# Optimization experiments

Hardware: AMD Instinct MI355X
Metric: run time of the kernel (lower is better)

## Reference

```python
import jax, jax.numpy as jnp
import numpy as np

B, C, H, W = 64, 768, 26, 26
M = 32
K_ATT = 192
NUM_CLASSES = 200
EPS = 1e-12


def setup_inputs() -> dict:
    key = jax.random.key(0)
    k1, k2, k3, k4, k5 = jax.random.split(key, 5)
    return {
        "feature_maps": jax.random.normal(k1, (B, C, H, W), dtype=jnp.float32),
        "att_w": jax.random.normal(k2, (K_ATT, C), dtype=jnp.float32) * 0.02,
        "att_b": jax.random.normal(k3, (K_ATT,), dtype=jnp.float32) * 0.02,
        "fc_w": jax.random.normal(k4, (NUM_CLASSES, M * C), dtype=jnp.float32) * 0.02,
        "fc_b": jax.random.normal(k5, (NUM_CLASSES,), dtype=jnp.float32) * 0.02,
    }


def reference(feature_maps, att_w, att_b, fc_w, fc_b):
    b, c, h, w = feature_maps.shape
    # 1x1 attention conv + relu, keep first M maps
    att = jax.nn.relu(
        jnp.einsum("bchw,kc->bkhw", feature_maps, att_w)
        + att_b[None, :, None, None]
    )
    att_m = att[:, :M]  # [B, M, H, W]

    # BAP: the Python loop multiply+avgpool+concat is a single batched contraction
    fm = jnp.einsum("bmhw,bchw->bmc", att_m, feature_maps) / (h * w)
    # signed sqrt
    fm = jnp.sign(fm) * jnp.sqrt(jnp.abs(fm) + EPS)
    # L2 normalize over dims (1, 2), matching F.normalize(eps=1e-12)
    nrm = jnp.sqrt(jnp.sum(fm * fm, axis=(1, 2), keepdims=True))
    fm = fm / jnp.maximum(nrm, EPS)

    # fc 1x1 conv on [B, M*C, 1, 1] == dense GEMM; input scaled by 100
    p = (fm.reshape(b, M * c) * 100.0) @ fc_w.T + fc_b
    return p, fm, att_m
```

## Files before the change

kernel.cpp:

```cpp
#include <hip/hip_runtime.h>
#include <hip/hip_bf16.h>


typedef unsigned short u16;
typedef __bf16 bf16x8_t __attribute__((ext_vector_type(8)));
typedef float f32x4_t __attribute__((ext_vector_type(4)));
typedef unsigned int uint32x4 __attribute__((ext_vector_type(4)));

union Frag { uint32x4 u4; unsigned u[4]; u16 s[8]; bf16x8_t v; };
union BFU { __hip_bfloat16 h; u16 u; };

__device__ inline u16 f2b(float x) { BFU t; t.h = __float2bfloat16(x); return t.u; }

__device__ inline void load8_cvt(const float* p, Frag& f) {
    f32x4_t x0 = *(const f32x4_t*)(p);
    f32x4_t x1 = *(const f32x4_t*)(p + 4);
#pragma unroll
    for (int j = 0; j < 4; ++j) { f.s[j] = f2b(x0[j]); f.s[4 + j] = f2b(x1[j]); }
}

#define MFMA(a, b, c) __builtin_amdgcn_mfma_f32_16x16x32_bf16((a), (b), (c), 0, 0, 0)

__global__ __launch_bounds__(256) void k_att(
    const float* __restrict__ fm, const float* __restrict__ att_w,
    const float* __restrict__ att_b, float* __restrict__ att_out,
    __hip_bfloat16* __restrict__ att_pad, float* __restrict__ p_sums)
{
    const int b  = blockIdx.y;
    const int p0 = blockIdx.x << 5;
    const int t  = threadIdx.x;
    const int wv = t >> 6, l = t & 63, q = l >> 4, ln = l & 15;

    if (blockIdx.x == 0 && t == 0) p_sums[b] = 0.f;

    __shared__ float red[32][32][4];

    f32x4_t acc[2][2] = {{{0.f,0.f,0.f,0.f},{0.f,0.f,0.f,0.f}},
                         {{0.f,0.f,0.f,0.f},{0.f,0.f,0.f,0.f}}};

    const int  kb   = wv * 192;
    const bool edge = (p0 == 672);
    const int  pb0  = p0 + ln;
    const int  pb1  = p0 + 16 + ln;

#pragma unroll
    for (int it = 0; it < 6; ++it) {
        const int k0 = kb + it * 32;
        Frag a0, a1, b0, b1;
        load8_cvt(att_w + (size_t)ln * 768 + k0 + q * 8, a0);
        load8_cvt(att_w + (size_t)(16 + ln) * 768 + k0 + q * 8, a1);
        const float* base = fm + (size_t)(b * 768 + k0 + q * 8) * 676;
        if (!edge) {
#pragma unroll
            for (int j = 0; j < 8; ++j) {
                b0.s[j] = f2b(base[(size_t)j * 676 + pb0]);
                b1.s[j] = f2b(base[(size_t)j * 676 + pb1]);
            }
        } else {
#pragma unroll
            for (int j = 0; j < 8; ++j) {
                b0.s[j] = (pb0 < 676) ? f2b(base[(size_t)j * 676 + pb0]) : (u16)0;
                b1.s[j] = (u16)0;
            }
        }
        acc[0][0] = MFMA(a0.v, b0.v, acc[0][0]);
        acc[0][1] = MFMA(a0.v, b1.v, acc[0][1]);
        acc[1][0] = MFMA(a1.v, b0.v, acc[1][0]);
        acc[1][1] = MFMA(a1.v, b1.v, acc[1][1]);
    }

#pragma unroll
    for (int mh = 0; mh < 2; ++mh)
#pragma unroll
        for (int ph = 0; ph < 2; ++ph)
#pragma unroll
            for (int r = 0; r < 4; ++r)
                red[mh * 16 + q * 4 + r][ph * 16 + ln][wv] = acc[mh][ph][r];
    __syncthreads();

    const int m = t >> 3, c0 = (t & 7) << 2;
#pragma unroll
    for (int j = 0; j < 4; ++j) {
        const int pl = c0 + j;
        f32x4_t v4 = *(const f32x4_t*)&red[m][pl][0];
        float v = v4[0] + v4[1] + v4[2] + v4[3] + att_b[m];
        v = v > 0.f ? v : 0.f;
        const int p = p0 + pl;
        BFU hb; hb.u = f2b(v);
        att_pad[(size_t)(b * 32 + m) * 704 + p] = (p < 676) ? hb.h : (__hip_bfloat16)0.f;
        if (p < 676)
            att_out[(size_t)(b * 32 + m) * 676 + p] = v;
    }
}

__global__ __launch_bounds__(256) void k_pool(
    const float* __restrict__ fm, const u16* __restrict__ att_pad,
    float* __restrict__ pooled, float* __restrict__ p_sums)
{
    const int b  = blockIdx.y;
    const int n0 = blockIdx.x << 5;
    const int t  = threadIdx.x;
    const int wv = t >> 6, l = t & 63, q = l >> 4, ln = l & 15;

    __shared__ float red[32][32][4];
    __shared__ float rs[4];

    const u16*   Ab = att_pad + (size_t)b * 32 * 704;
    const float* B0 = fm + (size_t)(b * 768 + n0 + ln) * 676;
    const float* B1 = fm + (size_t)(b * 768 + n0 + 16 + ln) * 676;

    f32x4_t acc[2][2] = {{{0.f,0.f,0.f,0.f},{0.f,0.f,0.f,0.f}},
                         {{0.f,0.f,0.f,0.f},{0.f,0.f,0.f,0.f}}};

    for (int it = wv; it < 22; it += 4) {
        const int k = it * 32 + q * 8;
        Frag a0, a1, b0, b1;
        a0.u4 = *(const uint32x4*)(Ab + (size_t)ln * 704 + k);
        a1.u4 = *(const uint32x4*)(Ab + (size_t)(16 + ln) * 704 + k);
        if (it < 21) {
            load8_cvt(B0 + k, b0);
            load8_cvt(B1 + k, b1);
        } else {
            b0.u[0]=0u; b0.u[1]=0u; b0.u[2]=0u; b0.u[3]=0u;
            b1.u[0]=0u; b1.u[1]=0u; b1.u[2]=0u; b1.u[3]=0u;
            if (q == 0) {
                f32x4_t x0 = *(const f32x4_t*)(B0 + 672);
                f32x4_t x1 = *(const f32x4_t*)(B1 + 672);
#pragma unroll
                for (int j = 0; j < 4; ++j) { b0.s[j] = f2b(x0[j]); b1.s[j] = f2b(x1[j]); }
            }
        }
        acc[0][0] = MFMA(a0.v, b0.v, acc[0][0]);
        acc[0][1] = MFMA(a0.v, b1.v, acc[0][1]);
        acc[1][0] = MFMA(a1.v, b0.v, acc[1][0]);
        acc[1][1] = MFMA(a1.v, b1.v, acc[1][1]);
    }

#pragma unroll
    for (int mh = 0; mh < 2; ++mh)
#pragma unroll
        for (int ch = 0; ch < 2; ++ch)
#pragma unroll
            for (int r = 0; r < 4; ++r)
                red[mh * 16 + q * 4 + r][ch * 16 + ln][wv] = acc[mh][ch][r];
    __syncthreads();

    const float sc = 1.0f / 676.0f;
    const int m = t >> 3, c0 = (t & 7) << 2;
    float ls = 0.f;
#pragma unroll
    for (int j = 0; j < 4; ++j) {
        const int cl = c0 + j;
        f32x4_t v4 = *(const f32x4_t*)&red[m][cl][0];
        float v = (v4[0] + v4[1] + v4[2] + v4[3]) * sc;
        pooled[(size_t)(b * 32 + m) * 768 + n0 + cl] = v;
        ls += fabsf(v);
    }
    for (int off = 32; off > 0; off >>= 1) ls += __shfl_down(ls, off);
    if (l == 0) rs[wv] = ls;
    __syncthreads();
    if (t == 0) atomicAdd(p_sums + b, rs[0] + rs[1] + rs[2] + rs[3]);
}

__global__ __launch_bounds__(256) void k_norm(
    const float* __restrict__ pooled, const float* __restrict__ p_sums,
    float* __restrict__ fm_out, u16* __restrict__ fmn16)
{
    const int b = blockIdx.x;
    const size_t base = (size_t)b * 24576 + (size_t)blockIdx.y * 2048;
    const float tot = p_sums[b] + 24576.f * 1e-12f;
    const float inv = 1.f / fmaxf(sqrtf(tot), 1e-12f);
    const int t = threadIdx.x;
#pragma unroll
    for (int i = 0; i < 8; ++i) {
        const size_t idx = base + i * 256 + t;
        float x = pooled[idx];
        float v = (x == 0.f) ? 0.f : copysignf(sqrtf(fabsf(x) + 1e-12f), x);
        float o = v * inv;
        fm_out[idx] = o;
        fmn16[idx]  = f2b(o);
    }
}

__global__ __launch_bounds__(256) void k_fc(
    const u16* __restrict__ fmn16, const float* __restrict__ fc_w,
    float* __restrict__ p_part)
{
    const int ntile = blockIdx.x;
    const int slab  = blockIdx.y;
    const int t = threadIdx.x;
    const int wv = t >> 6, l = t & 63, q = l >> 4, ln = l & 15;
    const int n = ntile * 16 + ln;
    const int kbase = slab * 512;

    const u16*   Ab = fmn16 + (size_t)(wv * 16 + ln) * 24576 + kbase + q * 8;
    const float* Bb = fc_w + (size_t)n * 24576 + kbase + q * 8;
    const bool nok = n < 200;

    f32x4_t acc = {0.f, 0.f, 0.f, 0.f};
#pragma unroll
    for (int kk = 0; kk < 512; kk += 32) {
        Frag af, bf2;
        af.u4 = *(const uint32x4*)(Ab + kk);
        if (nok) load8_cvt(Bb + kk, bf2);
        else { bf2.u[0] = 0u; bf2.u[1] = 0u; bf2.u[2] = 0u; bf2.u[3] = 0u; }
        acc = MFMA(af.v, bf2.v, acc);
    }
#pragma unroll
    for (int r = 0; r < 4; ++r) {
        const int bb = wv * 16 + q * 4 + r;
        p_part[(size_t)(slab * 64 + bb) * 208 + ntile * 16 + ln] = acc[r];
    }
}

__global__ __launch_bounds__(256) void k_fin(
    const float* __restrict__ p_part, const float* __restrict__ fc_b,
    float* __restrict__ p_out)
{
    const int tid = blockIdx.x * 256 + threadIdx.x;
    const int b = tid / 200, n = tid - b * 200;
    float s = 0.f;
#pragma unroll
    for (int sl = 0; sl < 48; ++sl) s += p_part[(size_t)(sl * 64 + b) * 208 + n];
    p_out[tid] = s * 100.f + fc_b[n];
}

extern "C" void kernel_launch(void* const* d_in, const int* in_sizes, int n_in,
                              void* d_out, int out_size, void* d_ws, size_t ws_size,
                              hipStream_t stream)
{
    const float* fm    = (const float*)d_in[0];
    const float* att_w = (const float*)d_in[1];
    const float* att_b = (const float*)d_in[2];
    const float* fc_w  = (const float*)d_in[3];
    const float* fc_b  = (const float*)d_in[4];

    float* out     = (float*)d_out;
    float* p_out   = out;
    float* fm_out  = out + 12800;
    float* att_out = out + 12800 + 64 * 32 * 768;

    char* ws = (char*)d_ws;
    __hip_bfloat16* att_pad = (__hip_bfloat16*)ws;
    float* p_part = (float*)ws;
    float* pooled = (float*)(ws + 2883584);
    u16*   fmn16  = (u16*)(ws + 2883584 + 6291456);
    float* p_sums = (float*)(ws + 2883584 + 6291456 + 3145728);

    k_att <<<dim3(22, 64), 256, 0, stream>>>(fm, att_w, att_b, att_out, att_pad, p_sums);
    k_pool<<<dim3(24, 64), 256, 0, stream>>>(fm, (const u16*)att_pad, pooled, p_sums);
    k_norm<<<dim3(64, 12), 256, 0, stream>>>(pooled, p_sums, fm_out, fmn16);
    k_fc  <<<dim3(13, 48), 256, 0, stream>>>(fmn16, fc_w, p_part);
    k_fin <<<dim3(50),     256, 0, stream>>>(p_part, fc_b, p_out);
}
```

Before: 274.3 us.

## Pre-convert feature maps to padded bf16 and widen attention tile

Adds a conversion kernel that writes the fp32 feature maps once as a padded bf16 buffer (row stride 704), which both the attention GEMM and the pooling GEMM then read instead of fp32 with per-element conversion and edge handling. The attention kernel now covers 64 spatial positions per block instead of 32, and its epilogue stores four values at a time with vector writes. In exchange it costs an extra full pass over the 133MB input plus a 69MB bf16 write and an extra launch. The later kernels read roughly half the bytes each, and k_att also gets more MFMA work per A-fragment load.

```diff
diff --git a/kernel.cpp b/kernel.cpp
--- a/kernel.cpp
+++ b/kernel.cpp
@@ -6,6 +6,7 @@
 typedef __bf16 bf16x8_t __attribute__((ext_vector_type(8)));
 typedef float f32x4_t __attribute__((ext_vector_type(4)));
 typedef unsigned int uint32x4 __attribute__((ext_vector_type(4)));
+typedef unsigned int uint32x2 __attribute__((ext_vector_type(2)));
 
 union Frag { uint32x4 u4; unsigned u[4]; u16 s[8]; bf16x8_t v; };
 union BFU { __hip_bfloat16 h; u16 u; };
@@ -21,80 +22,103 @@
 
 #define MFMA(a, b, c) __builtin_amdgcn_mfma_f32_16x16x32_bf16((a), (b), (c), 0, 0, 0)
 
+__global__ __launch_bounds__(256) void k_cvt(
+    const float* __restrict__ fm, u16* __restrict__ fmb16,
+    float* __restrict__ p_sums)
+{
+    const int tid = blockIdx.x * 256 + threadIdx.x;
+    if (blockIdx.x == 0 && threadIdx.x < 64) p_sums[threadIdx.x] = 0.f;
+    const int cp  = tid % 176;
+    const int row = tid / 176;
+    u16* dst = fmb16 + (size_t)row * 704 + cp * 4;
+    uint32x2 w;
+    if (cp < 169) {
+        f32x4_t x = *(const f32x4_t*)(fm + (size_t)row * 676 + cp * 4);
+        w[0] = (unsigned)f2b(x[0]) | ((unsigned)f2b(x[1]) << 16);
+        w[1] = (unsigned)f2b(x[2]) | ((unsigned)f2b(x[3]) << 16);
+    } else {
+        w[0] = 0u; w[1] = 0u;
+    }
+    *(uint32x2*)dst = w;
+}
+
 __global__ __launch_bounds__(256) void k_att(
-    const float* __restrict__ fm, const float* __restrict__ att_w,
+    const u16* __restrict__ fmb16, const float* __restrict__ att_w,
     const float* __restrict__ att_b, float* __restrict__ att_out,
-    __hip_bfloat16* __restrict__ att_pad, float* __restrict__ p_sums)
+    __hip_bfloat16* __restrict__ att_pad)
 {
     const int b  = blockIdx.y;
-    const int p0 = blockIdx.x << 5;
+    const int p0 = blockIdx.x << 6;
     const int t  = threadIdx.x;
     const int wv = t >> 6, l = t & 63, q = l >> 4, ln = l & 15;
 
-    if (blockIdx.x == 0 && t == 0) p_sums[b] = 0.f;
-
-    __shared__ float red[32][32][4];
-
-    f32x4_t acc[2][2] = {{{0.f,0.f,0.f,0.f},{0.f,0.f,0.f,0.f}},
-                         {{0.f,0.f,0.f,0.f},{0.f,0.f,0.f,0.f}}};
-
-    const int  kb   = wv * 192;
-    const bool edge = (p0 == 672);
-    const int  pb0  = p0 + ln;
-    const int  pb1  = p0 + 16 + ln;
+    __shared__ float red[32][64][4];
+
+    f32x4_t acc[2][4];
+#pragma unroll
+    for (int i = 0; i < 2; ++i)
+#pragma unroll
+        for (int j = 0; j < 4; ++j) acc[i][j] = f32x4_t{0.f, 0.f, 0.f, 0.f};
+
+    const int kb = wv * 192;
+    const u16* Bbase = fmb16 + (size_t)b * 768 * 704 + p0;
 
 #pragma unroll
     for (int it = 0; it < 6; ++it) {
         const int k0 = kb + it * 32;
-        Frag a0, a1, b0, b1;
+        Frag a0, a1, bf[4];
         load8_cvt(att_w + (size_t)ln * 768 + k0 + q * 8, a0);
         load8_cvt(att_w + (size_t)(16 + ln) * 768 + k0 + q * 8, a1);
-        const float* base = fm + (size_t)(b * 768 + k0 + q * 8) * 676;
-        if (!edge) {
-#pragma unroll
-            for (int j = 0; j < 8; ++j) {
-                b0.s[j] = f2b(base[(size_t)j * 676 + pb0]);
-                b1.s[j] = f2b(base[(size_t)j * 676 + pb1]);
-            }
-        } else {
-#pragma unroll
-            for (int j = 0; j < 8; ++j) {
-                b0.s[j] = (pb0 < 676) ? f2b(base[(size_t)j * 676 + pb0]) : (u16)0;
-                b1.s[j] = (u16)0;
-            }
+        const u16* bp = Bbase + (size_t)(k0 + q * 8) * 704 + ln;
+#pragma unroll
+        for (int pc = 0; pc < 4; ++pc)
+#pragma unroll
+            for (int j = 0; j < 8; ++j)
+                bf[pc].s[j] = bp[(size_t)j * 704 + pc * 16];
+#pragma unroll
+        for (int pc = 0; pc < 4; ++pc) {
+            acc[0][pc] = MFMA(a0.v, bf[pc].v, acc[0][pc]);
+            acc[1][pc] = MFMA(a1.v, bf[pc].v, acc[1][pc]);
         }
-        acc[0][0] = MFMA(a0.v, b0.v, acc[0][0]);
-        acc[0][1] = MFMA(a0.v, b1.v, acc[0][1]);
-        acc[1][0] = MFMA(a1.v, b0.v, acc[1][0]);
-        acc[1][1] = MFMA(a1.v, b1.v, acc[1][1]);
     }
 
 #pragma unroll
     for (int mh = 0; mh < 2; ++mh)
 #pragma unroll
-        for (int ph = 0; ph < 2; ++ph)
+        for (int pc = 0; pc < 4; ++pc)
 #pragma unroll
             for (int r = 0; r < 4; ++r)
-                red[mh * 16 + q * 4 + r][ph * 16 + ln][wv] = acc[mh][ph][r];
+                red[mh * 16 + q * 4 + r][pc * 16 + ln][wv] = acc[mh][pc][r];
     __syncthreads();
 
-    const int m = t >> 3, c0 = (t & 7) << 2;
-#pragma unroll
-    for (int j = 0; j < 4; ++j) {
-        const int pl = c0 + j;
-        f32x4_t v4 = *(const f32x4_t*)&red[m][pl][0];
-        float v = v4[0] + v4[1] + v4[2] + v4[3] + att_b[m];
-        v = v > 0.f ? v : 0.f;
-        const int p = p0 + pl;
-        BFU hb; hb.u = f2b(v);
-        att_pad[(size_t)(b * 32 + m) * 704 + p] = (p < 676) ? hb.h : (__hip_bfloat16)0.f;
-        if (p < 676)
-            att_out[(size_t)(b * 32 + m) * 676 + p] = v;
+    const int m  = t >> 3;
+    const int pg = (t & 7) << 3;
+    const float bias = att_b[m];
+#pragma unroll
+    for (int g = 0; g < 2; ++g) {
+        const int pl = pg + g * 4;
+        const int p  = p0 + pl;
+        f32x4_t v;
+        u16 h[4];
+#pragma unroll
+        for (int j = 0; j < 4; ++j) {
+            f32x4_t r4 = *(const f32x4_t*)&red[m][pl + j][0];
+            float x = r4[0] + r4[1] + r4[2] + r4[3] + bias;
+            x = x > 0.f ? x : 0.f;
+            v[j] = x;
+            h[j] = (p + j < 676) ? f2b(x) : (u16)0;
+        }
+        if (p <= 672)
+            *(f32x4_t*)(att_out + (size_t)(b * 32 + m) * 676 + p) = v;
+        uint32x2 w;
+        w[0] = (unsigned)h[0] | ((unsigned)h[1] << 16);
+        w[1] = (unsigned)h[2] | ((unsigned)h[3] << 16);
+        *(uint32x2*)((u16*)att_pad + (size_t)(b * 32 + m) * 704 + p) = w;
     }
 }
 
 __global__ __launch_bounds__(256) void k_pool(
-    const float* __restrict__ fm, const u16* __restrict__ att_pad,
+    const u16* __restrict__ fmb16, const u16* __restrict__ att_pad,
     float* __restrict__ pooled, float* __restrict__ p_sums)
 {
     const int b  = blockIdx.y;
@@ -105,9 +129,9 @@
     __shared__ float red[32][32][4];
     __shared__ float rs[4];
 
-    const u16*   Ab = att_pad + (size_t)b * 32 * 704;
-    const float* B0 = fm + (size_t)(b * 768 + n0 + ln) * 676;
-    const float* B1 = fm + (size_t)(b * 768 + n0 + 16 + ln) * 676;
+    const u16* Ab = att_pad + (size_t)b * 32 * 704;
+    const u16* B0 = fmb16 + (size_t)(b * 768 + n0 + ln) * 704;
+    const u16* B1 = fmb16 + (size_t)(b * 768 + n0 + 16 + ln) * 704;
 
     f32x4_t acc[2][2] = {{{0.f,0.f,0.f,0.f},{0.f,0.f,0.f,0.f}},
                          {{0.f,0.f,0.f,0.f},{0.f,0.f,0.f,0.f}}};
@@ -117,19 +141,8 @@
         Frag a0, a1, b0, b1;
         a0.u4 = *(const uint32x4*)(Ab + (size_t)ln * 704 + k);
         a1.u4 = *(const uint32x4*)(Ab + (size_t)(16 + ln) * 704 + k);
-        if (it < 21) {
-            load8_cvt(B0 + k, b0);
-            load8_cvt(B1 + k, b1);
-        } else {
-            b0.u[0]=0u; b0.u[1]=0u; b0.u[2]=0u; b0.u[3]=0u;
-            b1.u[0]=0u; b1.u[1]=0u; b1.u[2]=0u; b1.u[3]=0u;
-            if (q == 0) {
-                f32x4_t x0 = *(const f32x4_t*)(B0 + 672);
-                f32x4_t x1 = *(const f32x4_t*)(B1 + 672);
-#pragma unroll
-                for (int j = 0; j < 4; ++j) { b0.s[j] = f2b(x0[j]); b1.s[j] = f2b(x1[j]); }
-            }
-        }
+        b0.u4 = *(const uint32x4*)(B0 + k);
+        b1.u4 = *(const uint32x4*)(B1 + k);
         acc[0][0] = MFMA(a0.v, b0.v, acc[0][0]);
         acc[0][1] = MFMA(a0.v, b1.v, acc[0][1]);
         acc[1][0] = MFMA(a1.v, b0.v, acc[1][0]);
@@ -241,14 +254,16 @@
     float* att_out = out + 12800 + 64 * 32 * 768;
 
     char* ws = (char*)d_ws;
-    __hip_bfloat16* att_pad = (__hip_bfloat16*)ws;
-    float* p_part = (float*)ws;
-    float* pooled = (float*)(ws + 2883584);
-    u16*   fmn16  = (u16*)(ws + 2883584 + 6291456);
-    float* p_sums = (float*)(ws + 2883584 + 6291456 + 3145728);
-
-    k_att <<<dim3(22, 64), 256, 0, stream>>>(fm, att_w, att_b, att_out, att_pad, p_sums);
-    k_pool<<<dim3(24, 64), 256, 0, stream>>>(fm, (const u16*)att_pad, pooled, p_sums);
+    u16* fmb16 = (u16*)ws;
+    __hip_bfloat16* att_pad = (__hip_bfloat16*)(ws + 69206016);
+    float* p_part = (float*)(ws + 69206016);
+    float* pooled = (float*)(ws + 69206016 + 2883584);
+    u16*   fmn16  = (u16*)(ws + 69206016 + 2883584 + 6291456);
+    float* p_sums = (float*)(ws + 69206016 + 2883584 + 6291456 + 3145728);
+
+    k_cvt <<<dim3(33792), 256, 0, stream>>>(fm, fmb16, p_sums);
+    k_att <<<dim3(11, 64), 256, 0, stream>>>(fmb16, att_w, att_b, att_out, att_pad);
+    k_pool<<<dim3(24, 64), 256, 0, stream>>>(fmb16, (const u16*)att_pad, pooled, p_sums);
     k_norm<<<dim3(64, 12), 256, 0, stream>>>(pooled, p_sums, fm_out, fmn16);
     k_fc  <<<dim3(13, 48), 256, 0, stream>>>(fmn16, fc_w, p_part);
     k_fin <<<dim3(50),     256, 0, stream>>>(p_part, fc_b, p_out);
```

After: 279.1 us. No clear change (+1.8%).

## Stage feature tiles through double-buffered LDS with vector loads in attention kernel

Applied to the files above, without the earlier changes.

The attention conv kernel now covers 64 spatial positions per block instead of 32. Each thread does coalesced float4 loads of the feature map, converts them to bf16 and writes them into a double-buffered LDS tile, replacing the scattered per-element global gathers. The K reduction moves from a per-wave split of 192 channels to 128-channel chunks with the next chunk prefetched during compute. Outputs are written with vector stores, and p_sums is zeroed by a single block. This aims to reduce uncoalesced global traffic in the attention pass, at the cost of more LDS, extra barriers and a halved grid (11x64 blocks).

```diff
diff --git a/kernel.cpp b/kernel.cpp
--- a/kernel.cpp
+++ b/kernel.cpp
@@ -6,6 +6,7 @@
 typedef __bf16 bf16x8_t __attribute__((ext_vector_type(8)));
 typedef float f32x4_t __attribute__((ext_vector_type(4)));
 typedef unsigned int uint32x4 __attribute__((ext_vector_type(4)));
+typedef unsigned int uint32x2 __attribute__((ext_vector_type(2)));
 
 union Frag { uint32x4 u4; unsigned u[4]; u16 s[8]; bf16x8_t v; };
 union BFU { __hip_bfloat16 h; u16 u; };
@@ -24,73 +25,111 @@
 __global__ __launch_bounds__(256) void k_att(
     const float* __restrict__ fm, const float* __restrict__ att_w,
     const float* __restrict__ att_b, float* __restrict__ att_out,
-    __hip_bfloat16* __restrict__ att_pad, float* __restrict__ p_sums)
+    u16* __restrict__ att_pad, float* __restrict__ p_sums)
 {
     const int b  = blockIdx.y;
-    const int p0 = blockIdx.x << 5;
+    const int p0 = blockIdx.x << 6;
     const int t  = threadIdx.x;
     const int wv = t >> 6, l = t & 63, q = l >> 4, ln = l & 15;
 
-    if (blockIdx.x == 0 && t == 0) p_sums[b] = 0.f;
-
-    __shared__ float red[32][32][4];
-
-    f32x4_t acc[2][2] = {{{0.f,0.f,0.f,0.f},{0.f,0.f,0.f,0.f}},
-                         {{0.f,0.f,0.f,0.f},{0.f,0.f,0.f,0.f}}};
-
-    const int  kb   = wv * 192;
-    const bool edge = (p0 == 672);
-    const int  pb0  = p0 + ln;
-    const int  pb1  = p0 + 16 + ln;
-
-#pragma unroll
-    for (int it = 0; it < 6; ++it) {
-        const int k0 = kb + it * 32;
-        Frag a0, a1, b0, b1;
-        load8_cvt(att_w + (size_t)ln * 768 + k0 + q * 8, a0);
-        load8_cvt(att_w + (size_t)(16 + ln) * 768 + k0 + q * 8, a1);
-        const float* base = fm + (size_t)(b * 768 + k0 + q * 8) * 676;
-        if (!edge) {
-#pragma unroll
-            for (int j = 0; j < 8; ++j) {
-                b0.s[j] = f2b(base[(size_t)j * 676 + pb0]);
-                b1.s[j] = f2b(base[(size_t)j * 676 + pb1]);
-            }
+    if (blockIdx.x == 0 && b == 0 && t < 64) p_sums[t] = 0.f;
+
+    __shared__ u16 smem[2 * 8448];
+    float* red = (float*)smem;
+
+    const int  rr  = t >> 4;
+    const int  c4  = t & 15;
+    const bool cok = (p0 + c4 * 4 + 3) < 676;
+    const float* fbase = fm + (size_t)(b * 768) * 676 + p0 + c4 * 4;
+
+    f32x4_t pre[8];
+    f32x4_t acc[2][4];
+#pragma unroll
+    for (int i = 0; i < 2; ++i)
+#pragma unroll
+        for (int j = 0; j < 4; ++j) acc[i][j] = f32x4_t{0.f, 0.f, 0.f, 0.f};
+
+    auto loadf = [&](int c) {
+#pragma unroll
+        for (int i = 0; i < 8; ++i) {
+            const int r = rr + 16 * i;
+            pre[i] = cok ? *(const f32x4_t*)(fbase + (size_t)(c * 128 + r) * 676)
+                         : f32x4_t{0.f, 0.f, 0.f, 0.f};
+        }
+    };
+    auto commit = [&](int buf) {
+        u16* tp = smem + buf * 8448;
+#pragma unroll
+        for (int i = 0; i < 8; ++i) {
+            const int r = rr + 16 * i;
+            uint32x2 w;
+            w[0] = (unsigned)f2b(pre[i][0]) | ((unsigned)f2b(pre[i][1]) << 16);
+            w[1] = (unsigned)f2b(pre[i][2]) | ((unsigned)f2b(pre[i][3]) << 16);
+            *(uint32x2*)(tp + r * 66 + c4 * 4) = w;
+        }
+    };
+    auto compute = [&](int c, int buf) {
+        const u16* tp = smem + buf * 8448;
+        const int kk = c * 128 + wv * 32;
+        Frag a0, a1, bf[4];
+        load8_cvt(att_w + (size_t)ln * 768 + kk + q * 8, a0);
+        load8_cvt(att_w + (size_t)(16 + ln) * 768 + kk + q * 8, a1);
+        const u16* bp = tp + (wv * 32 + q * 8) * 66 + ln;
+#pragma unroll
+        for (int pc = 0; pc < 4; ++pc)
+#pragma unroll
+            for (int j = 0; j < 8; ++j)
+                bf[pc].s[j] = bp[j * 66 + pc * 16];
+#pragma unroll
+        for (int pc = 0; pc < 4; ++pc) {
+            acc[0][pc] = MFMA(a0.v, bf[pc].v, acc[0][pc]);
+            acc[1][pc] = MFMA(a1.v, bf[pc].v, acc[1][pc]);
+        }
+    };
+
+    loadf(0); commit(0); __syncthreads();
+#pragma unroll
+    for (int c = 0; c < 6; ++c) {
+        if (c < 5) loadf(c + 1);
+        compute(c, c & 1);
+        if (c < 5) { commit((c + 1) & 1); __syncthreads(); }
+    }
+    __syncthreads();
+
+#pragma unroll
+    for (int mh = 0; mh < 2; ++mh)
+#pragma unroll
+        for (int pc = 0; pc < 4; ++pc)
+#pragma unroll
+            for (int r = 0; r < 4; ++r)
+                red[((mh * 16 + q * 4 + r) * 64 + pc * 16 + ln) * 4 + wv] = acc[mh][pc][r];
+    __syncthreads();
+
+    const int m = t >> 3, pl0 = (t & 7) << 3;
+    const float bias = att_b[m];
+    Frag hw;
+#pragma unroll
+    for (int g = 0; g < 2; ++g) {
+        f32x4_t v;
+#pragma unroll
+        for (int j = 0; j < 4; ++j) {
+            const int pl = pl0 + g * 4 + j;
+            f32x4_t r4 = *(const f32x4_t*)&red[(m * 64 + pl) * 4];
+            float x = r4[0] + r4[1] + r4[2] + r4[3] + bias;
+            x = x > 0.f ? x : 0.f;
+            v[j] = x;
+            hw.s[g * 4 + j] = (p0 + pl < 676) ? f2b(x) : (u16)0;
+        }
+        const int p = p0 + pl0 + g * 4;
+        if (p + 3 < 676) {
+            *(f32x4_t*)(att_out + (size_t)(b * 32 + m) * 676 + p) = v;
         } else {
 #pragma unroll
-            for (int j = 0; j < 8; ++j) {
-                b0.s[j] = (pb0 < 676) ? f2b(base[(size_t)j * 676 + pb0]) : (u16)0;
-                b1.s[j] = (u16)0;
-            }
-        }
-        acc[0][0] = MFMA(a0.v, b0.v, acc[0][0]);
-        acc[0][1] = MFMA(a0.v, b1.v, acc[0][1]);
-        acc[1][0] = MFMA(a1.v, b0.v, acc[1][0]);
-        acc[1][1] = MFMA(a1.v, b1.v, acc[1][1]);
-    }
-
-#pragma unroll
-    for (int mh = 0; mh < 2; ++mh)
-#pragma unroll
-        for (int ph = 0; ph < 2; ++ph)
-#pragma unroll
-            for (int r = 0; r < 4; ++r)
-                red[mh * 16 + q * 4 + r][ph * 16 + ln][wv] = acc[mh][ph][r];
-    __syncthreads();
-
-    const int m = t >> 3, c0 = (t & 7) << 2;
-#pragma unroll
-    for (int j = 0; j < 4; ++j) {
-        const int pl = c0 + j;
-        f32x4_t v4 = *(const f32x4_t*)&red[m][pl][0];
-        float v = v4[0] + v4[1] + v4[2] + v4[3] + att_b[m];
-        v = v > 0.f ? v : 0.f;
-        const int p = p0 + pl;
-        BFU hb; hb.u = f2b(v);
-        att_pad[(size_t)(b * 32 + m) * 704 + p] = (p < 676) ? hb.h : (__hip_bfloat16)0.f;
-        if (p < 676)
-            att_out[(size_t)(b * 32 + m) * 676 + p] = v;
-    }
+            for (int j = 0; j < 4; ++j)
+                if (p + j < 676) att_out[(size_t)(b * 32 + m) * 676 + p + j] = v[j];
+        }
+    }
+    *(uint32x4*)(att_pad + (size_t)(b * 32 + m) * 704 + p0 + pl0) = hw.u4;
 }
 
 __global__ __launch_bounds__(256) void k_pool(
@@ -241,14 +280,14 @@
     float* att_out = out + 12800 + 64 * 32 * 768;
 
     char* ws = (char*)d_ws;
-    __hip_bfloat16* att_pad = (__hip_bfloat16*)ws;
-    float* p_part = (float*)ws;
-    float* pooled = (float*)(ws + 2883584);
-    u16*   fmn16  = (u16*)(ws + 2883584 + 6291456);
-    float* p_sums = (float*)(ws + 2883584 + 6291456 + 3145728);
-
-    k_att <<<dim3(22, 64), 256, 0, stream>>>(fm, att_w, att_b, att_out, att_pad, p_sums);
-    k_pool<<<dim3(24, 64), 256, 0, stream>>>(fm, (const u16*)att_pad, pooled, p_sums);
+    u16*   att_pad = (u16*)ws;
+    float* p_part  = (float*)ws;
+    float* pooled  = (float*)(ws + 2883584);
+    u16*   fmn16   = (u16*)(ws + 2883584 + 6291456);
+    float* p_sums  = (float*)(ws + 2883584 + 6291456 + 3145728);
+
+    k_att <<<dim3(11, 64), 256, 0, stream>>>(fm, att_w, att_b, att_out, att_pad, p_sums);
+    k_pool<<<dim3(24, 64), 256, 0, stream>>>(fm, att_pad, pooled, p_sums);
     k_norm<<<dim3(64, 12), 256, 0, stream>>>(pooled, p_sums, fm_out, fmn16);
     k_fc  <<<dim3(13, 48), 256, 0, stream>>>(fmn16, fc_w, p_part);
     k_fin <<<dim3(50),     256, 0, stream>>>(p_part, fc_b, p_out);
```

Result: faster. 260.2 us (-5.1%).
